# Performance work log

Hardware: AMD Instinct MI355X
Metric: run time of the kernel (lower is better)

Reference implementation:

```python
import jax, jax.numpy as jnp
import numpy as np
import math

N, C_IN, H, W = 8, 256, 64, 64
C_ATT, C_OUT = 128, 256
BN_EPS = 1e-5


def conv_bn_relu(x, w, gamma, beta, mean, var):
    # 1x1 conv (no bias) + BatchNorm (eval mode) + ReLU
    y = jnp.einsum('oc,nchw->nohw', w, x)
    inv = gamma / jnp.sqrt(var + BN_EPS)
    y = y * inv[None, :, None, None] + (beta - mean * inv)[None, :, None, None]
    return jax.nn.relu(y)


def setup_inputs() -> dict:
    key = jax.random.key(0)
    ks = jax.random.split(key, 12)
    x = jax.random.normal(ks[0], (N, C_IN, H, W), dtype=jnp.float32)
    mask = jnp.ones((N, 1, H, W), dtype=jnp.float32)
    reduc_w = jax.random.normal(ks[1], (C_OUT, C_IN), dtype=jnp.float32) * (1.0 / math.sqrt(C_IN))
    reduc_gamma = jnp.ones((C_OUT,), dtype=jnp.float32)
    reduc_beta = jnp.zeros((C_OUT,), dtype=jnp.float32)
    reduc_mean = jax.random.normal(ks[2], (C_OUT,), dtype=jnp.float32) * 0.1
    reduc_var = jax.random.uniform(ks[3], (C_OUT,), dtype=jnp.float32) + 0.5
    att_w = jax.random.normal(ks[4], (C_ATT, C_IN), dtype=jnp.float32) * (1.0 / math.sqrt(C_IN))
    att_gamma = jnp.ones((C_ATT,), dtype=jnp.float32)
    att_beta = jnp.zeros((C_ATT,), dtype=jnp.float32)
    att_mean = jax.random.normal(ks[5], (C_ATT,), dtype=jnp.float32) * 0.1
    att_var = jax.random.uniform(ks[6], (C_ATT,), dtype=jnp.float32) + 0.5
    return {
        'x': x, 'mask': mask,
        'reduc_w': reduc_w, 'reduc_gamma': reduc_gamma, 'reduc_beta': reduc_beta,
        'reduc_mean': reduc_mean, 'reduc_var': reduc_var,
        'att_w': att_w, 'att_gamma': att_gamma, 'att_beta': att_beta,
        'att_mean': att_mean, 'att_var': att_var,
    }


def reference(x, mask, reduc_w, reduc_gamma, reduc_beta, reduc_mean, reduc_var,
              att_w, att_gamma, att_beta, att_mean, att_var):
    n, _, h, w = x.shape
    x_feat = conv_bn_relu(x, reduc_w, reduc_gamma, reduc_beta, reduc_mean, reduc_var)   # [n,C_OUT,h,w]
    x_atten = conv_bn_relu(x, att_w, att_gamma, att_beta, att_mean, att_var)            # [n,C_ATT,h,w]
    c = x_atten.shape[1]
    q = x_atten.reshape(n, c, h * w)                                                    # [n,c,HW]
    # energy[n,i,j] = sum_c q[n,c,i]*q[n,c,j] / (1e-8 + sqrt(c))
    energy = jnp.einsum('nci,ncj->nij', q, q) / (1e-8 + math.sqrt(c))
    energy = energy + (mask.reshape(n, 1, h * w) - 1.0) * 1e8
    weight = jax.nn.softmax(energy, axis=2)                                             # [n,HW,HW]
    feat = x_feat.reshape(n, x_feat.shape[1], h * w)                                    # [n,C_OUT,HW]
    out = jnp.einsum('nij,ncj->nci', weight, feat)                                      # [n,C_OUT,HW]
    out = out.reshape(n, feat.shape[1], h, w)
    out = out * mask
    return out
```

## Files before the change

kernel.cpp:

```cpp
#include <hip/hip_runtime.h>
#include <cstdint>
#include <cstddef>

#define NB 8
#define CIN 256
#define HWX 4096
#define CF 256
#define CA 128
#define CT 384

typedef __attribute__((ext_vector_type(8))) _Float16 half8;
typedef __attribute__((ext_vector_type(8))) short short8;
typedef __attribute__((ext_vector_type(4))) short s16x4;
typedef __attribute__((ext_vector_type(4))) float f32x4;
typedef __attribute__((ext_vector_type(4))) unsigned int u32x4;
typedef __attribute__((ext_vector_type(2))) unsigned int u32x2;

#define OFF_WH   0
#define OFF_BIAS (CT*CIN*2)
#define OFF_FEAT (OFF_BIAS + CT*4)
#define OFF_Q    (OFF_FEAT + NB*CF*HWX*2)
#define OFF_NORM (OFF_Q + NB*HWX*CA*2)
#define OFF_G    (OFF_NORM + NB*HWX*4)

__device__ inline unsigned short f16_bits(float f) {
  _Float16 h = (_Float16)f;
  return __builtin_bit_cast(unsigned short, h);
}
__device__ inline half8 ld_half8(const unsigned short* p) {
  short8 r = *(const short8*)p;
  return __builtin_bit_cast(half8, r);
}

__device__ inline void g2l16(const void* g, void* l) {
  __builtin_amdgcn_global_load_lds(
      (const __attribute__((address_space(1))) unsigned int*)g,
      (__attribute__((address_space(3))) unsigned int*)l, 16, 0, 0);
}

__global__ __launch_bounds__(256) void fold_bn_k(
    const float* __restrict__ rw, const float* __restrict__ rg,
    const float* __restrict__ rb, const float* __restrict__ rm, const float* __restrict__ rv,
    const float* __restrict__ aw, const float* __restrict__ ag,
    const float* __restrict__ ab2, const float* __restrict__ am, const float* __restrict__ av,
    unsigned short* __restrict__ wh, float* __restrict__ bias, unsigned* __restrict__ Gmax) {
  int o = blockIdx.x, k = threadIdx.x;
  if (o == 0 && k < NB) Gmax[k] = 0u;
  const float* wsrc; float g, b, m, v;
  if (o < CF) { wsrc = rw + (size_t)o*CIN; g = rg[o]; b = rb[o]; m = rm[o]; v = rv[o]; }
  else { int oa = o - CF; wsrc = aw + (size_t)oa*CIN; g = ag[oa]; b = ab2[oa]; m = am[oa]; v = av[oa]; }
  float inv = g / sqrtf(v + 1e-5f);
  wh[(size_t)o*CIN + k] = f16_bits(wsrc[k] * inv);
  if (k == 0) bias[o] = b - m*inv;
}

__global__ __launch_bounds__(512, 4) void conv_k(
    const float* __restrict__ x, const unsigned short* __restrict__ wh,
    const float* __restrict__ bias, unsigned short* __restrict__ feat,
    unsigned short* __restrict__ q, float* __restrict__ normq,
    unsigned* __restrict__ Gmax) {
  __shared__ unsigned short sX[64*256];
  unsigned short (*sQr)[136] = (unsigned short(*)[136])sX;
  int b = blockIdx.x;
  int n = b & 7, pt0 = b >> 3;
  int p0 = pt0 * 64;
  int t = threadIdx.x;
  int w = t >> 6, lane = t & 63, quad = lane >> 4, col = lane & 15;
  const float* xn = x + (size_t)n*CIN*HWX;

  #pragma unroll
  for (int pass=0; pass<4; pass++) {
    int idx = pass*512 + t;
    int kp = idx >> 4, c4 = idx & 15;
    f32x4 a = *(const f32x4*)(xn + (size_t)(2*kp)*HWX + p0 + c4*4);
    f32x4 c = *(const f32x4*)(xn + (size_t)(2*kp+1)*HWX + p0 + c4*4);
    int unit = kp >> 2, off = kp & 3;
    #pragma unroll
    for (int j=0;j<4;j++) {
      int pos = c4*4 + j;
      unsigned dd = (unsigned)f16_bits(a[j]) | ((unsigned)f16_bits(c[j]) << 16);
      *(unsigned*)&sX[pos*256 + ((unit ^ (pos & 31)) << 3) + off*2] = dd;
    }
  }
  __syncthreads();

  f32x4 fzero = {0.f,0.f,0.f,0.f};
  f32x4 acc[4][3];
  #pragma unroll
  for (int pt=0;pt<4;pt++)
    #pragma unroll
    for (int ot=0;ot<3;ot++) acc[pt][ot] = fzero;

  int ocb = w*48;
  #pragma unroll
  for (int ks=0; ks<8; ks++) {
    half8 B3[3];
    #pragma unroll
    for (int ot=0;ot<3;ot++)
      B3[ot] = ld_half8(wh + (size_t)(ocb + ot*16 + col)*CIN + ks*32 + quad*8);
    half8 A4[4];
    #pragma unroll
    for (int pt=0;pt<4;pt++) {
      int pos = pt*16 + col;
      A4[pt] = ld_half8(&sX[pos*256 + (((ks*4 + quad) ^ (pos & 31)) << 3)]);
    }
    #pragma unroll
    for (int pt=0;pt<4;pt++)
      #pragma unroll
      for (int ot=0;ot<3;ot++)
        acc[pt][ot] = __builtin_amdgcn_mfma_f32_16x16x32_f16(A4[pt], B3[ot], acc[pt][ot], 0, 0, 0);
  }
  __syncthreads();

  float bv[3];
  #pragma unroll
  for (int ot=0;ot<3;ot++) bv[ot] = bias[ocb + ot*16 + col];
  #pragma unroll
  for (int pt=0;pt<4;pt++)
    #pragma unroll
    for (int ot=0;ot<3;ot++) {
      int oc = ocb + ot*16 + col;
      alignas(8) unsigned short u4[4];
      #pragma unroll
      for (int r=0;r<4;r++)
        u4[r] = f16_bits(fmaxf(acc[pt][ot][r] + bv[ot], 0.f));
      if (oc < CF) {
        *(u32x2*)(feat + (size_t)n*CF*HWX + (size_t)oc*HWX + p0 + pt*16 + quad*4) =
            *(const u32x2*)u4;
      } else {
        int cc = oc - CF;
        #pragma unroll
        for (int r=0;r<4;r++)
          sQr[pt*16 + quad*4 + r][cc] = u4[r];
      }
    }
  __syncthreads();

  if (t < 256) {
    int pos = t >> 2, seg = t & 3;
    const unsigned short* src = &sQr[pos][seg*32];
    unsigned short* dst = q + ((size_t)n*HWX + p0 + pos)*CA + seg*32;
    float s2 = 0.f;
    #pragma unroll
    for (int u=0;u<4;u++) {
      short8 v = *(const short8*)(src + u*8);
      *(short8*)(dst + u*8) = v;
      half8 h = __builtin_bit_cast(half8, v);
      #pragma unroll
      for (int e=0;e<8;e++) { float fe = (float)h[e]; s2 += fe*fe; }
    }
    s2 += __shfl_xor(s2, 1, 64);
    s2 += __shfl_xor(s2, 2, 64);
    if (seg == 0) normq[(size_t)n*HWX + p0 + pos] = sqrtf(s2);
    float mx = s2;
    mx = fmaxf(mx, __shfl_xor(mx, 4, 64));
    mx = fmaxf(mx, __shfl_xor(mx, 8, 64));
    mx = fmaxf(mx, __shfl_xor(mx, 16, 64));
    mx = fmaxf(mx, __shfl_xor(mx, 32, 64));
    if (lane == 0) atomicMax(Gmax + n, __float_as_uint(sqrtf(mx)));
  }
}

__global__ __launch_bounds__(512, 4) void flash_k(
    const unsigned short* __restrict__ q, const unsigned short* __restrict__ feat,
    const float* __restrict__ mask, const float* __restrict__ normq,
    const unsigned* __restrict__ Gmax, float* __restrict__ out) {
  __shared__ alignas(16) unsigned short sQ[128*128];
  __shared__ alignas(16) unsigned short sP[64][132];
  __shared__ float sM[128];
  __shared__ float sL[2][64];
  int b = blockIdx.x;
  int n = b & 7, it = b >> 3;
  int i0 = it * 64;
  int t = threadIdx.x;
  int w = t >> 6, lane = t & 63, quad = lane >> 4, col = lane & 15;
  int wq = w & 3, wh = w >> 2;
  const unsigned short* q_n = q + (size_t)n*HWX*CA;
  const unsigned short* f_n = feat + (size_t)n*CF*HWX;
  const float* m_n = mask + (size_t)n*HWX;
  const int rloc = t >> 4 & 31, oct16 = t & 15;
  const float inv_s = 1.0f/(1e-8f + sqrtf(128.0f));

  auto stage_Q = [&](int j0) {
    #pragma unroll
    for (int c=0;c<4;c++) {
      int row = c*32 + rloc;
      int og = oct16 ^ (row & 15);
      g2l16(q_n + (size_t)(j0+row)*CA + og*8, &sQ[(size_t)row*128 + oct16*8]);
    }
    if (t < 32) g2l16(m_n + j0 + t*4, &sM[t*4]);
  };

  half8 ah[4];
  {
    int arow = i0 + wq*16 + col;
    #pragma unroll
    for (int ks=0; ks<4; ks++)
      ah[ks] = ld_half8(q_n + (size_t)arow*CA + ks*32 + quad*8);
  }
  float Gn = __uint_as_float(Gmax[n]);
  float cvals[4];
  #pragma unroll
  for (int r=0;r<4;r++)
    cvals[r] = normq[(size_t)n*HWX + i0 + wq*16 + quad*4 + r] * Gn * inv_s - 5.0f;

  f32x4 fzero = {0.f,0.f,0.f,0.f};
  f32x4 o[4][2];
  #pragma unroll
  for (int ig=0;ig<4;ig++) { o[ig][0] = fzero; o[ig][1] = fzero; }
  float lrun[4] = {0.f,0.f,0.f,0.f};

  stage_Q(0);
  #pragma unroll 1
  for (int ji = 0; ji < 32; ji++) {
    int j0 = ji*128;
    __syncthreads();

    half8 bF01[2][2];
    #pragma unroll
    for (int ks2=0;ks2<2;ks2++)
      #pragma unroll
      for (int ct=0;ct<2;ct++) {
        int c = w*32 + ct*16 + col;
        bF01[ks2][ct] = ld_half8(f_n + (size_t)c*HWX + j0 + ks2*32 + quad*8);
      }

    f32x4 s[4];
    #pragma unroll
    for (int jt=0;jt<4;jt++) s[jt] = fzero;
    __builtin_amdgcn_s_setprio(1);
    #pragma unroll
    for (int jt=0;jt<4;jt++) {
      int rowj = wh*64 + jt*16 + col;
      #pragma unroll
      for (int ks=0; ks<4; ks++) {
        int slot = (ks*4 + quad) ^ (rowj & 15);
        half8 bq = ld_half8(&sQ[rowj*128 + slot*8]);
        s[jt] = __builtin_amdgcn_mfma_f32_16x16x32_f16(ah[ks], bq, s[jt], 0, 0, 0);
      }
    }
    __builtin_amdgcn_s_setprio(0);

    #pragma unroll
    for (int jt=0;jt<4;jt++) {
      float mj = (sM[wh*64 + jt*16 + col] - 1.f) * 1e8f;
      #pragma unroll
      for (int r=0;r<4;r++) {
        float p = __expf(s[jt][r]*inv_s + mj - cvals[r]);
        lrun[r] += p;
        sP[wq*16 + quad*4 + r][wh*64 + jt*16 + col] = f16_bits(p);
      }
    }

    __syncthreads();
    if (ji + 1 < 32) stage_Q(j0+128);

    half8 bF23[2][2];
    #pragma unroll
    for (int ks2=0;ks2<2;ks2++)
      #pragma unroll
      for (int ct=0;ct<2;ct++) {
        int c = w*32 + ct*16 + col;
        bF23[ks2][ct] = ld_half8(f_n + (size_t)c*HWX + j0 + (ks2+2)*32 + quad*8);
      }
    __builtin_amdgcn_s_setprio(1);
    #pragma unroll
    for (int ks2=0; ks2<4; ks2++) {
      half8 aP[4];
      #pragma unroll
      for (int ig=0;ig<4;ig++) {
        const unsigned short* pp = &sP[ig*16 + col][ks2*32 + quad*8];
        s16x4 lo = *(const s16x4*)pp;
        s16x4 hi = *(const s16x4*)(pp + 4);
        short8 vv = __builtin_shufflevector(lo, hi, 0,1,2,3,4,5,6,7);
        aP[ig] = __builtin_bit_cast(half8, vv);
      }
      #pragma unroll
      for (int ct=0;ct<2;ct++) {
        half8 bF = (ks2 < 2) ? bF01[ks2][ct] : bF23[ks2-2][ct];
        #pragma unroll
        for (int ig=0;ig<4;ig++)
          o[ig][ct] = __builtin_amdgcn_mfma_f32_16x16x32_f16(aP[ig], bF, o[ig][ct], 0, 0, 0);
      }
    }
    __builtin_amdgcn_s_setprio(0);
  }

  #pragma unroll
  for (int r=0;r<4;r++) {
    float ss = lrun[r];
    ss += __shfl_xor(ss, 1, 64);
    ss += __shfl_xor(ss, 2, 64);
    ss += __shfl_xor(ss, 4, 64);
    ss += __shfl_xor(ss, 8, 64);
    lrun[r] = ss;
  }
  #pragma unroll
  for (int r=0;r<4;r++)
    if (col == 0) sL[wh][wq*16 + quad*4 + r] = lrun[r];
  __syncthreads();
  #pragma unroll
  for (int ig=0;ig<4;ig++) {
    int base = ig*16 + quad*4;
    f32x4 l0 = *(const f32x4*)&sL[0][base];
    f32x4 l1 = *(const f32x4*)&sL[1][base];
    f32x4 mv = *(const f32x4*)(m_n + i0 + base);
    f32x4 minv;
    #pragma unroll
    for (int r=0;r<4;r++) minv[r] = mv[r] / (l0[r] + l1[r]);
    #pragma unroll
    for (int ct=0;ct<2;ct++) {
      int c = w*32 + ct*16 + col;
      f32x4 v;
      #pragma unroll
      for (int r=0;r<4;r++) v[r] = o[ig][ct][r] * minv[r];
      *(f32x4*)(out + ((size_t)n*CF + c)*HWX + i0 + base) = v;
    }
  }
}

extern "C" void kernel_launch(void* const* d_in, const int* in_sizes, int n_in,
                              void* d_out, int out_size, void* d_ws, size_t ws_size,
                              hipStream_t stream) {
  const float* x    = (const float*)d_in[0];
  const float* mask = (const float*)d_in[1];
  const float* rw   = (const float*)d_in[2];
  const float* rg   = (const float*)d_in[3];
  const float* rb   = (const float*)d_in[4];
  const float* rm   = (const float*)d_in[5];
  const float* rv   = (const float*)d_in[6];
  const float* aw   = (const float*)d_in[7];
  const float* ag   = (const float*)d_in[8];
  const float* ab   = (const float*)d_in[9];
  const float* am   = (const float*)d_in[10];
  const float* av   = (const float*)d_in[11];
  float* out = (float*)d_out;
  char* ws = (char*)d_ws;
  unsigned short* wh = (unsigned short*)(ws + OFF_WH);
  float* bias = (float*)(ws + OFF_BIAS);
  unsigned short* feat = (unsigned short*)(ws + OFF_FEAT);
  unsigned short* q    = (unsigned short*)(ws + OFF_Q);
  float* normq = (float*)(ws + OFF_NORM);
  unsigned* Gmax = (unsigned*)(ws + OFF_G);

  hipLaunchKernelGGL(fold_bn_k, dim3(CT), dim3(CIN), 0, stream,
                     rw, rg, rb, rm, rv, aw, ag, ab, am, av, wh, bias, Gmax);
  hipLaunchKernelGGL(conv_k, dim3(512), dim3(512), 0, stream,
                     x, wh, bias, feat, q, normq, Gmax);
  hipLaunchKernelGGL(flash_k, dim3(512), dim3(512), 0, stream,
                     q, feat, mask, normq, Gmax, out);
}
```

Baseline: 294.2 us.

## Retile flash score computation 2x2 per warp, prefetch conv weights, batch Gmax atomics

The flash kernel's QK^T stage is retiled so each warp computes a 32x32 score block (two query row tiles by two key tiles) instead of 16x64. Each loaded shared-memory Q fragment now feeds two MFMAs, which halves LDS reads in that stage at the cost of more registers for the extra query fragments and row sums. The row-sum reduction grows to four partial buffers. The conv kernel also prefetches the next k-slice of weights (software double-buffering) and reduces the per-block max norm in shared memory before one atomicMax, cutting global atomics per block.

```diff
diff --git a/kernel.cpp b/kernel.cpp
--- a/kernel.cpp
+++ b/kernel.cpp
@@ -60,6 +60,7 @@
     unsigned short* __restrict__ q, float* __restrict__ normq,
     unsigned* __restrict__ Gmax) {
   __shared__ unsigned short sX[64*256];
+  __shared__ float sGm[4];
   unsigned short (*sQr)[136] = (unsigned short(*)[136])sX;
   int b = blockIdx.x;
   int n = b & 7, pt0 = b >> 3;
@@ -92,12 +93,18 @@
     for (int ot=0;ot<3;ot++) acc[pt][ot] = fzero;
 
   int ocb = w*48;
+  half8 B3[3];
+  #pragma unroll
+  for (int ot=0;ot<3;ot++)
+    B3[ot] = ld_half8(wh + (size_t)(ocb + ot*16 + col)*CIN + quad*8);
   #pragma unroll
   for (int ks=0; ks<8; ks++) {
-    half8 B3[3];
-    #pragma unroll
-    for (int ot=0;ot<3;ot++)
-      B3[ot] = ld_half8(wh + (size_t)(ocb + ot*16 + col)*CIN + ks*32 + quad*8);
+    half8 B3n[3];
+    if (ks < 7) {
+      #pragma unroll
+      for (int ot=0;ot<3;ot++)
+        B3n[ot] = ld_half8(wh + (size_t)(ocb + ot*16 + col)*CIN + (ks+1)*32 + quad*8);
+    }
     half8 A4[4];
     #pragma unroll
     for (int pt=0;pt<4;pt++) {
@@ -109,6 +116,10 @@
       #pragma unroll
       for (int ot=0;ot<3;ot++)
         acc[pt][ot] = __builtin_amdgcn_mfma_f32_16x16x32_f16(A4[pt], B3[ot], acc[pt][ot], 0, 0, 0);
+    if (ks < 7) {
+      #pragma unroll
+      for (int ot=0;ot<3;ot++) B3[ot] = B3n[ot];
+    }
   }
   __syncthreads();
 
@@ -157,7 +168,13 @@
     mx = fmaxf(mx, __shfl_xor(mx, 8, 64));
     mx = fmaxf(mx, __shfl_xor(mx, 16, 64));
     mx = fmaxf(mx, __shfl_xor(mx, 32, 64));
-    if (lane == 0) atomicMax(Gmax + n, __float_as_uint(sqrtf(mx)));
+    if (lane == 0) sGm[t >> 6] = sqrtf(mx);
+  }
+  __syncthreads();
+  if (t == 0) {
+    float m01 = fmaxf(sGm[0], sGm[1]);
+    float m23 = fmaxf(sGm[2], sGm[3]);
+    atomicMax(Gmax + n, __float_as_uint(fmaxf(m01, m23)));
   }
 }
 
@@ -168,13 +185,13 @@
   __shared__ alignas(16) unsigned short sQ[128*128];
   __shared__ alignas(16) unsigned short sP[64][132];
   __shared__ float sM[128];
-  __shared__ float sL[2][64];
+  __shared__ float sL[4][64];
   int b = blockIdx.x;
   int n = b & 7, it = b >> 3;
   int i0 = it * 64;
   int t = threadIdx.x;
   int w = t >> 6, lane = t & 63, quad = lane >> 4, col = lane & 15;
-  int wq = w & 3, wh = w >> 2;
+  int wiq = w & 1, wjq = w >> 1;
   const unsigned short* q_n = q + (size_t)n*HWX*CA;
   const unsigned short* f_n = feat + (size_t)n*CF*HWX;
   const float* m_n = mask + (size_t)n*HWX;
@@ -191,24 +208,27 @@
     if (t < 32) g2l16(m_n + j0 + t*4, &sM[t*4]);
   };
 
-  half8 ah[4];
-  {
-    int arow = i0 + wq*16 + col;
+  half8 ah[2][4];
+  #pragma unroll
+  for (int ip=0; ip<2; ip++) {
+    int arow = i0 + wiq*32 + ip*16 + col;
     #pragma unroll
     for (int ks=0; ks<4; ks++)
-      ah[ks] = ld_half8(q_n + (size_t)arow*CA + ks*32 + quad*8);
+      ah[ip][ks] = ld_half8(q_n + (size_t)arow*CA + ks*32 + quad*8);
   }
   float Gn = __uint_as_float(Gmax[n]);
-  float cvals[4];
-  #pragma unroll
-  for (int r=0;r<4;r++)
-    cvals[r] = normq[(size_t)n*HWX + i0 + wq*16 + quad*4 + r] * Gn * inv_s - 5.0f;
+  float cvals[2][4];
+  #pragma unroll
+  for (int ip=0;ip<2;ip++)
+    #pragma unroll
+    for (int r=0;r<4;r++)
+      cvals[ip][r] = normq[(size_t)n*HWX + i0 + wiq*32 + ip*16 + quad*4 + r] * Gn * inv_s - 5.0f;
 
   f32x4 fzero = {0.f,0.f,0.f,0.f};
   f32x4 o[4][2];
   #pragma unroll
   for (int ig=0;ig<4;ig++) { o[ig][0] = fzero; o[ig][1] = fzero; }
-  float lrun[4] = {0.f,0.f,0.f,0.f};
+  float lrun[2][4] = {{0.f,0.f,0.f,0.f},{0.f,0.f,0.f,0.f}};
 
   stage_Q(0);
   #pragma unroll 1
@@ -225,31 +245,34 @@
         bF01[ks2][ct] = ld_half8(f_n + (size_t)c*HWX + j0 + ks2*32 + quad*8);
       }
 
-    f32x4 s[4];
-    #pragma unroll
-    for (int jt=0;jt<4;jt++) s[jt] = fzero;
+    f32x4 s[2][2];
+    s[0][0] = fzero; s[0][1] = fzero; s[1][0] = fzero; s[1][1] = fzero;
     __builtin_amdgcn_s_setprio(1);
     #pragma unroll
-    for (int jt=0;jt<4;jt++) {
-      int rowj = wh*64 + jt*16 + col;
+    for (int jt=0;jt<2;jt++) {
+      int rowj = wjq*32 + jt*16 + col;
       #pragma unroll
       for (int ks=0; ks<4; ks++) {
         int slot = (ks*4 + quad) ^ (rowj & 15);
         half8 bq = ld_half8(&sQ[rowj*128 + slot*8]);
-        s[jt] = __builtin_amdgcn_mfma_f32_16x16x32_f16(ah[ks], bq, s[jt], 0, 0, 0);
+        #pragma unroll
+        for (int ip=0;ip<2;ip++)
+          s[ip][jt] = __builtin_amdgcn_mfma_f32_16x16x32_f16(ah[ip][ks], bq, s[ip][jt], 0, 0, 0);
       }
     }
     __builtin_amdgcn_s_setprio(0);
 
     #pragma unroll
-    for (int jt=0;jt<4;jt++) {
-      float mj = (sM[wh*64 + jt*16 + col] - 1.f) * 1e8f;
-      #pragma unroll
-      for (int r=0;r<4;r++) {
-        float p = __expf(s[jt][r]*inv_s + mj - cvals[r]);
-        lrun[r] += p;
-        sP[wq*16 + quad*4 + r][wh*64 + jt*16 + col] = f16_bits(p);
-      }
+    for (int jt=0;jt<2;jt++) {
+      float mj = (sM[wjq*32 + jt*16 + col] - 1.f) * 1e8f;
+      #pragma unroll
+      for (int ip=0;ip<2;ip++)
+        #pragma unroll
+        for (int r=0;r<4;r++) {
+          float p = __expf(s[ip][jt][r]*inv_s + mj - cvals[ip][r]);
+          lrun[ip][r] += p;
+          sP[wiq*32 + ip*16 + quad*4 + r][wjq*32 + jt*16 + col] = f16_bits(p);
+        }
     }
 
     __syncthreads();
@@ -287,27 +310,28 @@
   }
 
   #pragma unroll
-  for (int r=0;r<4;r++) {
-    float ss = lrun[r];
-    ss += __shfl_xor(ss, 1, 64);
-    ss += __shfl_xor(ss, 2, 64);
-    ss += __shfl_xor(ss, 4, 64);
-    ss += __shfl_xor(ss, 8, 64);
-    lrun[r] = ss;
-  }
-  #pragma unroll
-  for (int r=0;r<4;r++)
-    if (col == 0) sL[wh][wq*16 + quad*4 + r] = lrun[r];
+  for (int ip=0;ip<2;ip++)
+    #pragma unroll
+    for (int r=0;r<4;r++) {
+      float ss = lrun[ip][r];
+      ss += __shfl_xor(ss, 1, 64);
+      ss += __shfl_xor(ss, 2, 64);
+      ss += __shfl_xor(ss, 4, 64);
+      ss += __shfl_xor(ss, 8, 64);
+      if (col == 0) sL[wjq][wiq*32 + ip*16 + quad*4 + r] = ss;
+    }
   __syncthreads();
   #pragma unroll
   for (int ig=0;ig<4;ig++) {
     int base = ig*16 + quad*4;
     f32x4 l0 = *(const f32x4*)&sL[0][base];
     f32x4 l1 = *(const f32x4*)&sL[1][base];
+    f32x4 l2 = *(const f32x4*)&sL[2][base];
+    f32x4 l3 = *(const f32x4*)&sL[3][base];
     f32x4 mv = *(const f32x4*)(m_n + i0 + base);
     f32x4 minv;
     #pragma unroll
-    for (int r=0;r<4;r++) minv[r] = mv[r] / (l0[r] + l1[r]);
+    for (int r=0;r<4;r++) minv[r] = mv[r] / (l0[r] + l1[r] + l2[r] + l3[r]);
     #pragma unroll
     for (int ct=0;ct<2;ct++) {
       int c = w*32 + ct*16 + col;
```

After: 389.4 us. +32.4%, slower.
